# Kernel optimization log

Measured on AMD Instinct MI355X. Metric: run time of the kernel, lower is better.

The kernel has to match this reference:

```python
import jax, jax.numpy as jnp
import numpy as np

B, T, H, IN = 64, 2048, 256, 6
TH_X = 0.0  # DeltaJANET hard-codes thx=0 into the rnn layer
TH_H = 0.0


def setup_inputs() -> dict:
    key = jax.random.key(0)
    ks = jax.random.split(key, 4)
    return {
        "x": jax.random.normal(ks[0], (B, T, 2), dtype=jnp.float32),
        "h_0": jnp.zeros((1, B, H), dtype=jnp.float32),
        "weight_ih": jax.random.normal(ks[1], (2 * H, IN), dtype=jnp.float32) * 0.2,
        "weight_hh": jax.random.normal(ks[2], (2 * H, H), dtype=jnp.float32) * 0.05,
        "bias_ih": jnp.zeros((2 * H,), dtype=jnp.float32),
        "bias_hh": jnp.zeros((2 * H,), dtype=jnp.float32),
        "fc_w": jax.random.normal(ks[3], (2, H), dtype=jnp.float32) * 0.05,
        "fc_b": jnp.zeros((2,), dtype=jnp.float32),
    }


def _features(x):
    i_x = x[..., 0:1]
    q_x = x[..., 1:2]
    amp = jnp.sqrt(i_x * i_x + q_x * q_x)
    amp3 = amp ** 3
    cos = i_x / amp
    sin = q_x / amp
    return jnp.concatenate((i_x, q_x, amp, amp3, sin, cos), axis=-1)  # [B,T,6]


def reference(x, h_0, weight_ih, weight_hh, bias_ih, bias_hh, fc_w, fc_b):
    feats = _features(x)                       # [B,T,6]
    xs = jnp.swapaxes(feats, 0, 1)             # [T,B,6] time-major
    b = x.shape[0]
    h0 = jnp.zeros((b, H), feats.dtype)        # h_0 arg is ignored (set to None in torch forward)
    dm0 = jnp.broadcast_to(bias_ih + bias_hh, (b, 2 * H)).astype(feats.dtype)
    x_p0 = jnp.zeros((b, IN), feats.dtype)

    def step(carry, x_t):
        x_p, h, h_p, dm = carry
        dx_raw = x_t - x_p
        dh_raw = h - h_p
        dx_abs = jnp.abs(dx_raw)
        dh_abs = jnp.abs(dh_raw)
        dx = jnp.where(dx_abs < TH_X, 0.0, dx_raw)
        dh = jnp.where(dh_abs < TH_H, 0.0, dh_raw)
        x_p_n = jnp.where(dx_abs >= TH_X, x_t, x_p)
        h_p_n = jnp.where(dh_abs >= TH_H, h, h_p)
        mac_x = dx @ weight_ih.T + dm           # [B,2H]
        mac_h = dh @ weight_hh.T                # [B,2H]
        dm_f = mac_x[:, :H] + mac_h[:, :H]
        dm_g = mac_x[:, H:] + mac_h[:, H:]
        dm_n = jnp.concatenate((dm_f, dm_g), axis=1)
        gate_f = jax.nn.sigmoid(dm_f)
        gate_g = jax.nn.sigmoid(dm_g)
        h_n = (1.0 - gate_f) * gate_g + gate_f * h
        return (x_p_n, h_n, h_p_n, dm_n), h_n

    _, hs = jax.lax.scan(step, (x_p0, h0, h0, dm0), xs)  # hs: [T,B,H]
    out = jnp.swapaxes(hs, 0, 1)               # [B,T,H]
    return out @ fc_w.T + fc_b                 # [B,T,2]
```

## Files before the change

kernel.cpp:

```cpp
#include <hip/hip_runtime.h>
#include <math.h>

typedef _Float16 half2v __attribute__((ext_vector_type(2)));

#define TT 2048
#define HP 36

#if __has_builtin(__builtin_amdgcn_fdot2)
#define FDOT2(a,b,c) __builtin_amdgcn_fdot2((a),(b),(c),false)
#else
#define FDOT2(a,b,c) ((c) + (float)(a).x*(float)(b).x + (float)(a).y*(float)(b).y)
#endif

__global__ __launch_bounds__(512)
__attribute__((amdgpu_waves_per_eu(2, 2)))
void janet_rnn(const float* __restrict__ x,
               const float* __restrict__ w_ih,
               const float* __restrict__ w_hh,
               const float* __restrict__ b_ih,
               const float* __restrict__ b_hh,
               const float* __restrict__ fc_w,
               const float* __restrict__ fc_b,
               float* __restrict__ out)
{
    __shared__ unsigned int hbuf[2][4 * HP];
    __shared__ float dm[512];
    __shared__ float wih[6][512];
    __shared__ float biasv[512];

    const int tid = threadIdx.x;
    const int b   = blockIdx.x;
    const int cc  = tid & 3;
    const int rg  = tid >> 2;
    const int r0  = rg * 4;
    const int c0  = cc * 64;

    if (tid < 4 * HP) { hbuf[0][tid] = 0u; hbuf[1][tid] = 0u; }
    biasv[tid] = b_ih[tid] + b_hh[tid];
    #pragma unroll
    for (int c = 0; c < 6; ++c) wih[c][tid] = w_ih[tid * 6 + c];

    half2v wp[4][32];
    #pragma unroll
    for (int i = 0; i < 4; ++i) {
        const float* wr = w_hh + (r0 + i) * 256 + c0;
        #pragma unroll
        for (int j = 0; j < 16; ++j) {
            const float4 v = *reinterpret_cast<const float4*>(wr + j * 4);
            half2v p0; p0.x = (_Float16)v.x; p0.y = (_Float16)v.y;
            half2v p1; p1.x = (_Float16)v.z; p1.y = (_Float16)v.w;
            wp[i][j * 2 + 0] = p0;
            wp[i][j * 2 + 1] = p1;
        }
    }

    const int pl = tid - 256;
    float fw[8];
    if (pl >= 0 && pl < 64) {
        #pragma unroll
        for (int k = 0; k < 4; ++k) {
            fw[k]     = fc_w[pl * 4 + k];
            fw[4 + k] = fc_w[256 + pl * 4 + k];
        }
    }
    const float fcb0 = fc_b[0], fcb1 = fc_b[1];

    float hreg = 0.0f;

    const float* xb   = x   + (size_t)b * TT * 2;
    float*       outb = out + (size_t)b * TT * 2;

    __syncthreads();

    #pragma unroll 1
    for (int t = 0; t < TT; ++t) {
        float xi = 0.f, xq = 0.f;
        if (tid < 256) {
            const float2 xv = *reinterpret_cast<const float2*>(xb + 2 * t);
            xi = xv.x; xq = xv.y;
        }

        const unsigned int* hb = &hbuf[(t + 1) & 1][cc * HP];
        half2v hr[32];
        #pragma unroll
        for (int q = 0; q < 8; ++q) {
            const uint4 r = *reinterpret_cast<const uint4*>(hb + 4 * q);
            hr[q * 4 + 0] = __builtin_bit_cast(half2v, r.x);
            hr[q * 4 + 1] = __builtin_bit_cast(half2v, r.y);
            hr[q * 4 + 2] = __builtin_bit_cast(half2v, r.z);
            hr[q * 4 + 3] = __builtin_bit_cast(half2v, r.w);
        }
        float a0 = 0.f, a1 = 0.f, a2 = 0.f, a3 = 0.f;
        #pragma unroll
        for (int j = 0; j < 32; ++j) {
            a0 = FDOT2(wp[0][j], hr[j], a0);
            a1 = FDOT2(wp[1][j], hr[j], a1);
            a2 = FDOT2(wp[2][j], hr[j], a2);
            a3 = FDOT2(wp[3][j], hr[j], a3);
        }
        a0 += __shfl_xor(a0, 1); a0 += __shfl_xor(a0, 2);
        a1 += __shfl_xor(a1, 1); a1 += __shfl_xor(a1, 2);
        a2 += __shfl_xor(a2, 1); a2 += __shfl_xor(a2, 2);
        a3 += __shfl_xor(a3, 1); a3 += __shfl_xor(a3, 2);
        if (cc == 0)
            *reinterpret_cast<float4*>(&dm[r0]) = make_float4(a0, a1, a2, a3);
        __syncthreads();

        if (tid < 256) {
            const float amp  = sqrtf(xi * xi + xq * xq);
            const float amp3 = amp * amp * amp;
            const float snv  = xq / amp;
            const float csv  = xi / amp;
            float dmf = dm[tid]       + biasv[tid];
            float dmg = dm[256 + tid] + biasv[256 + tid];
            dmf += wih[0][tid] * xi  + wih[1][tid] * xq  + wih[2][tid] * amp
                 + wih[3][tid] * amp3 + wih[4][tid] * snv + wih[5][tid] * csv;
            dmg += wih[0][256 + tid] * xi  + wih[1][256 + tid] * xq
                 + wih[2][256 + tid] * amp + wih[3][256 + tid] * amp3
                 + wih[4][256 + tid] * snv + wih[5][256 + tid] * csv;
            const float gf = 1.0f / (1.0f + __expf(-dmf));
            const float gg = 1.0f / (1.0f + __expf(-dmg));
            hreg = (1.0f - gf) * gg + gf * hreg;
            const float hhi = __shfl_down(hreg, 1);
            if ((tid & 1) == 0) {
                half2v hp2; hp2.x = (_Float16)hreg; hp2.y = (_Float16)hhi;
                const int c = tid >> 6;
                const int i = (tid >> 1) & 31;
                hbuf[t & 1][c * HP + i] = __builtin_bit_cast(unsigned int, hp2);
            }
        } else if (pl < 64 && t > 0) {
            const unsigned int* hp = hbuf[(t + 1) & 1];
            const int c = pl >> 4;
            const int i = (2 * pl) & 31;
            const unsigned int u0 = hp[c * HP + i];
            const unsigned int u1 = hp[c * HP + i + 1];
            const half2v ha = __builtin_bit_cast(half2v, u0);
            const half2v hc = __builtin_bit_cast(half2v, u1);
            const float h0v = (float)ha.x, h1v = (float)ha.y;
            const float h2v = (float)hc.x, h3v = (float)hc.y;
            float po0 = fw[0] * h0v + fw[1] * h1v + fw[2] * h2v + fw[3] * h3v;
            float po1 = fw[4] * h0v + fw[5] * h1v + fw[6] * h2v + fw[7] * h3v;
            #pragma unroll
            for (int s = 1; s < 64; s <<= 1) {
                po0 += __shfl_xor(po0, s);
                po1 += __shfl_xor(po1, s);
            }
            if (pl == 0)
                *reinterpret_cast<float2*>(outb + (t - 1) * 2) =
                    make_float2(po0 + fcb0, po1 + fcb1);
        }
        __syncthreads();
    }

    if (pl >= 0 && pl < 64) {
        const unsigned int* hp = hbuf[(TT - 1) & 1];
        const int c = pl >> 4;
        const int i = (2 * pl) & 31;
        const unsigned int u0 = hp[c * HP + i];
        const unsigned int u1 = hp[c * HP + i + 1];
        const half2v ha = __builtin_bit_cast(half2v, u0);
        const half2v hc = __builtin_bit_cast(half2v, u1);
        const float h0v = (float)ha.x, h1v = (float)ha.y;
        const float h2v = (float)hc.x, h3v = (float)hc.y;
        float po0 = fw[0] * h0v + fw[1] * h1v + fw[2] * h2v + fw[3] * h3v;
        float po1 = fw[4] * h0v + fw[5] * h1v + fw[6] * h2v + fw[7] * h3v;
        #pragma unroll
        for (int s = 1; s < 64; s <<= 1) {
            po0 += __shfl_xor(po0, s);
            po1 += __shfl_xor(po1, s);
        }
        if (pl == 0)
            *reinterpret_cast<float2*>(outb + (TT - 1) * 2) =
                make_float2(po0 + fcb0, po1 + fcb1);
    }
}

extern "C" void kernel_launch(void* const* d_in, const int* in_sizes, int n_in,
                              void* d_out, int out_size, void* d_ws, size_t ws_size,
                              hipStream_t stream) {
    (void)in_sizes; (void)n_in; (void)out_size; (void)d_ws; (void)ws_size;
    const float* x    = (const float*)d_in[0];
    const float* w_ih = (const float*)d_in[2];
    const float* w_hh = (const float*)d_in[3];
    const float* b_ih = (const float*)d_in[4];
    const float* b_hh = (const float*)d_in[5];
    const float* fc_w = (const float*)d_in[6];
    const float* fc_b = (const float*)d_in[7];
    float* outp = (float*)d_out;

    hipLaunchKernelGGL(janet_rnn, dim3(64), dim3(512), 0, stream,
                       x, w_ih, w_hh, b_ih, b_hh, fc_w, fc_b, outp);
}
```

Before: 2.445 ms.

## Split recurrent matvec across 1024 threads with 8-way column partition

Doubles the block to 1024 threads so each thread handles 32 columns of W_hh (8-way split) instead of 64, halving the serial dot-product chain per step and adding one more shuffle-reduction level. The input weights and bias move from shared memory into per-thread registers, fc weights go to shared memory, and the h buffer padding changes to 20 words per chunk. The cost is more waves synchronising at each of the two per-step barriers, plus an extra shuffle stage.

```diff
diff --git a/kernel.cpp b/kernel.cpp
--- a/kernel.cpp
+++ b/kernel.cpp
@@ -4,7 +4,7 @@
 typedef _Float16 half2v __attribute__((ext_vector_type(2)));
 
 #define TT 2048
-#define HP 36
+#define CH 20
 
 #if __has_builtin(__builtin_amdgcn_fdot2)
 #define FDOT2(a,b,c) __builtin_amdgcn_fdot2((a),(b),(c),false)
@@ -12,8 +12,7 @@
 #define FDOT2(a,b,c) ((c) + (float)(a).x*(float)(b).x + (float)(a).y*(float)(b).y)
 #endif
 
-__global__ __launch_bounds__(512)
-__attribute__((amdgpu_waves_per_eu(2, 2)))
+__global__ __launch_bounds__(1024, 4)
 void janet_rnn(const float* __restrict__ x,
                const float* __restrict__ w_ih,
                const float* __restrict__ w_hh,
@@ -23,29 +22,26 @@
                const float* __restrict__ fc_b,
                float* __restrict__ out)
 {
-    __shared__ unsigned int hbuf[2][4 * HP];
+    __shared__ unsigned int hbuf[2][8 * CH];
     __shared__ float dm[512];
-    __shared__ float wih[6][512];
-    __shared__ float biasv[512];
+    __shared__ float fcw[512];
 
     const int tid = threadIdx.x;
     const int b   = blockIdx.x;
-    const int cc  = tid & 3;
-    const int rg  = tid >> 2;
+    const int cc  = tid & 7;
+    const int rg  = tid >> 3;
     const int r0  = rg * 4;
-    const int c0  = cc * 64;
+    const int c0  = cc * 32;
 
-    if (tid < 4 * HP) { hbuf[0][tid] = 0u; hbuf[1][tid] = 0u; }
-    biasv[tid] = b_ih[tid] + b_hh[tid];
-    #pragma unroll
-    for (int c = 0; c < 6; ++c) wih[c][tid] = w_ih[tid * 6 + c];
+    if (tid < 8 * CH) { hbuf[0][tid] = 0u; hbuf[1][tid] = 0u; }
+    if (tid < 512) fcw[tid] = fc_w[tid];
 
-    half2v wp[4][32];
+    half2v wp[4][16];
     #pragma unroll
     for (int i = 0; i < 4; ++i) {
         const float* wr = w_hh + (r0 + i) * 256 + c0;
         #pragma unroll
-        for (int j = 0; j < 16; ++j) {
+        for (int j = 0; j < 8; ++j) {
             const float4 v = *reinterpret_cast<const float4*>(wr + j * 4);
             half2v p0; p0.x = (_Float16)v.x; p0.y = (_Float16)v.y;
             half2v p1; p1.x = (_Float16)v.z; p1.y = (_Float16)v.w;
@@ -54,15 +50,17 @@
         }
     }
 
+    float wf[6], wg[6], bsf = 0.f, bsg = 0.f;
+    if (tid < 256) {
+        #pragma unroll
+        for (int c = 0; c < 6; ++c) {
+            wf[c] = w_ih[tid * 6 + c];
+            wg[c] = w_ih[(256 + tid) * 6 + c];
+        }
+        bsf = b_ih[tid]       + b_hh[tid];
+        bsg = b_ih[256 + tid] + b_hh[256 + tid];
+    }
     const int pl = tid - 256;
-    float fw[8];
-    if (pl >= 0 && pl < 64) {
-        #pragma unroll
-        for (int k = 0; k < 4; ++k) {
-            fw[k]     = fc_w[pl * 4 + k];
-            fw[4 + k] = fc_w[256 + pl * 4 + k];
-        }
-    }
     const float fcb0 = fc_b[0], fcb1 = fc_b[1];
 
     float hreg = 0.0f;
@@ -80,28 +78,28 @@
             xi = xv.x; xq = xv.y;
         }
 
-        const unsigned int* hb = &hbuf[(t + 1) & 1][cc * HP];
-        half2v hr[32];
-        #pragma unroll
-        for (int q = 0; q < 8; ++q) {
-            const uint4 r = *reinterpret_cast<const uint4*>(hb + 4 * q);
-            hr[q * 4 + 0] = __builtin_bit_cast(half2v, r.x);
-            hr[q * 4 + 1] = __builtin_bit_cast(half2v, r.y);
-            hr[q * 4 + 2] = __builtin_bit_cast(half2v, r.z);
-            hr[q * 4 + 3] = __builtin_bit_cast(half2v, r.w);
-        }
+        const unsigned int* hb = &hbuf[(t + 1) & 1][cc * CH];
         float a0 = 0.f, a1 = 0.f, a2 = 0.f, a3 = 0.f;
         #pragma unroll
-        for (int j = 0; j < 32; ++j) {
-            a0 = FDOT2(wp[0][j], hr[j], a0);
-            a1 = FDOT2(wp[1][j], hr[j], a1);
-            a2 = FDOT2(wp[2][j], hr[j], a2);
-            a3 = FDOT2(wp[3][j], hr[j], a3);
+        for (int q = 0; q < 4; ++q) {
+            const uint4 r = *reinterpret_cast<const uint4*>(hb + 4 * q);
+            const half2v h0 = __builtin_bit_cast(half2v, r.x);
+            const half2v h1 = __builtin_bit_cast(half2v, r.y);
+            const half2v h2 = __builtin_bit_cast(half2v, r.z);
+            const half2v h3 = __builtin_bit_cast(half2v, r.w);
+            a0 = FDOT2(wp[0][q*4+0], h0, a0); a0 = FDOT2(wp[0][q*4+1], h1, a0);
+            a0 = FDOT2(wp[0][q*4+2], h2, a0); a0 = FDOT2(wp[0][q*4+3], h3, a0);
+            a1 = FDOT2(wp[1][q*4+0], h0, a1); a1 = FDOT2(wp[1][q*4+1], h1, a1);
+            a1 = FDOT2(wp[1][q*4+2], h2, a1); a1 = FDOT2(wp[1][q*4+3], h3, a1);
+            a2 = FDOT2(wp[2][q*4+0], h0, a2); a2 = FDOT2(wp[2][q*4+1], h1, a2);
+            a2 = FDOT2(wp[2][q*4+2], h2, a2); a2 = FDOT2(wp[2][q*4+3], h3, a2);
+            a3 = FDOT2(wp[3][q*4+0], h0, a3); a3 = FDOT2(wp[3][q*4+1], h1, a3);
+            a3 = FDOT2(wp[3][q*4+2], h2, a3); a3 = FDOT2(wp[3][q*4+3], h3, a3);
         }
-        a0 += __shfl_xor(a0, 1); a0 += __shfl_xor(a0, 2);
-        a1 += __shfl_xor(a1, 1); a1 += __shfl_xor(a1, 2);
-        a2 += __shfl_xor(a2, 1); a2 += __shfl_xor(a2, 2);
-        a3 += __shfl_xor(a3, 1); a3 += __shfl_xor(a3, 2);
+        a0 += __shfl_xor(a0, 1); a0 += __shfl_xor(a0, 2); a0 += __shfl_xor(a0, 4);
+        a1 += __shfl_xor(a1, 1); a1 += __shfl_xor(a1, 2); a1 += __shfl_xor(a1, 4);
+        a2 += __shfl_xor(a2, 1); a2 += __shfl_xor(a2, 2); a2 += __shfl_xor(a2, 4);
+        a3 += __shfl_xor(a3, 1); a3 += __shfl_xor(a3, 2); a3 += __shfl_xor(a3, 4);
         if (cc == 0)
             *reinterpret_cast<float4*>(&dm[r0]) = make_float4(a0, a1, a2, a3);
         __syncthreads();
@@ -111,35 +109,31 @@
             const float amp3 = amp * amp * amp;
             const float snv  = xq / amp;
             const float csv  = xi / amp;
-            float dmf = dm[tid]       + biasv[tid];
-            float dmg = dm[256 + tid] + biasv[256 + tid];
-            dmf += wih[0][tid] * xi  + wih[1][tid] * xq  + wih[2][tid] * amp
-                 + wih[3][tid] * amp3 + wih[4][tid] * snv + wih[5][tid] * csv;
-            dmg += wih[0][256 + tid] * xi  + wih[1][256 + tid] * xq
-                 + wih[2][256 + tid] * amp + wih[3][256 + tid] * amp3
-                 + wih[4][256 + tid] * snv + wih[5][256 + tid] * csv;
+            float dmf = dm[tid]       + bsf;
+            float dmg = dm[256 + tid] + bsg;
+            dmf += wf[0]*xi + wf[1]*xq + wf[2]*amp + wf[3]*amp3 + wf[4]*snv + wf[5]*csv;
+            dmg += wg[0]*xi + wg[1]*xq + wg[2]*amp + wg[3]*amp3 + wg[4]*snv + wg[5]*csv;
             const float gf = 1.0f / (1.0f + __expf(-dmf));
             const float gg = 1.0f / (1.0f + __expf(-dmg));
             hreg = (1.0f - gf) * gg + gf * hreg;
             const float hhi = __shfl_down(hreg, 1);
             if ((tid & 1) == 0) {
                 half2v hp2; hp2.x = (_Float16)hreg; hp2.y = (_Float16)hhi;
-                const int c = tid >> 6;
-                const int i = (tid >> 1) & 31;
-                hbuf[t & 1][c * HP + i] = __builtin_bit_cast(unsigned int, hp2);
+                const int d = tid >> 1;
+                hbuf[t & 1][(d >> 4) * CH + (d & 15)] =
+                    __builtin_bit_cast(unsigned int, hp2);
             }
         } else if (pl < 64 && t > 0) {
             const unsigned int* hp = hbuf[(t + 1) & 1];
-            const int c = pl >> 4;
-            const int i = (2 * pl) & 31;
-            const unsigned int u0 = hp[c * HP + i];
-            const unsigned int u1 = hp[c * HP + i + 1];
-            const half2v ha = __builtin_bit_cast(half2v, u0);
-            const half2v hc = __builtin_bit_cast(half2v, u1);
+            const int d0 = 2 * pl, d1 = 2 * pl + 1;
+            const half2v ha = __builtin_bit_cast(half2v, hp[(d0 >> 4) * CH + (d0 & 15)]);
+            const half2v hc = __builtin_bit_cast(half2v, hp[(d1 >> 4) * CH + (d1 & 15)]);
             const float h0v = (float)ha.x, h1v = (float)ha.y;
             const float h2v = (float)hc.x, h3v = (float)hc.y;
-            float po0 = fw[0] * h0v + fw[1] * h1v + fw[2] * h2v + fw[3] * h3v;
-            float po1 = fw[4] * h0v + fw[5] * h1v + fw[6] * h2v + fw[7] * h3v;
+            const float4 w0 = *reinterpret_cast<const float4*>(&fcw[4 * pl]);
+            const float4 w1 = *reinterpret_cast<const float4*>(&fcw[256 + 4 * pl]);
+            float po0 = w0.x*h0v + w0.y*h1v + w0.z*h2v + w0.w*h3v;
+            float po1 = w1.x*h0v + w1.y*h1v + w1.z*h2v + w1.w*h3v;
             #pragma unroll
             for (int s = 1; s < 64; s <<= 1) {
                 po0 += __shfl_xor(po0, s);
@@ -154,16 +148,15 @@
 
     if (pl >= 0 && pl < 64) {
         const unsigned int* hp = hbuf[(TT - 1) & 1];
-        const int c = pl >> 4;
-        const int i = (2 * pl) & 31;
-        const unsigned int u0 = hp[c * HP + i];
-        const unsigned int u1 = hp[c * HP + i + 1];
-        const half2v ha = __builtin_bit_cast(half2v, u0);
-        const half2v hc = __builtin_bit_cast(half2v, u1);
+        const int d0 = 2 * pl, d1 = 2 * pl + 1;
+        const half2v ha = __builtin_bit_cast(half2v, hp[(d0 >> 4) * CH + (d0 & 15)]);
+        const half2v hc = __builtin_bit_cast(half2v, hp[(d1 >> 4) * CH + (d1 & 15)]);
         const float h0v = (float)ha.x, h1v = (float)ha.y;
         const float h2v = (float)hc.x, h3v = (float)hc.y;
-        float po0 = fw[0] * h0v + fw[1] * h1v + fw[2] * h2v + fw[3] * h3v;
-        float po1 = fw[4] * h0v + fw[5] * h1v + fw[6] * h2v + fw[7] * h3v;
+        const float4 w0 = *reinterpret_cast<const float4*>(&fcw[4 * pl]);
+        const float4 w1 = *reinterpret_cast<const float4*>(&fcw[256 + 4 * pl]);
+        float po0 = w0.x*h0v + w0.y*h1v + w0.z*h2v + w0.w*h3v;
+        float po1 = w1.x*h0v + w1.y*h1v + w1.z*h2v + w1.w*h3v;
         #pragma unroll
         for (int s = 1; s < 64; s <<= 1) {
             po0 += __shfl_xor(po0, s);
@@ -188,6 +181,6 @@
     const float* fc_b = (const float*)d_in[7];
     float* outp = (float*)d_out;
 
-    hipLaunchKernelGGL(janet_rnn, dim3(64), dim3(512), 0, stream,
+    hipLaunchKernelGGL(janet_rnn, dim3(64), dim3(1024), 0, stream,
                        x, w_ih, w_hh, b_ih, b_hh, fc_w, fc_b, outp);
 }
```

Result: slower. 2.904 ms (+18.8%).
